# Optimization experiments

Measured on AMD Instinct MI355X. Metric: run time of the kernel, lower is better.

Reference implementation:

```python
import jax, jax.numpy as jnp
import numpy as np

B, L, D, T = 32, 512, 1024, 256
MAX_MENTION_LEN = 10
NEG_INF = float('-inf')


def _static_bounds_and_keep():
    # Full (start, end) grid, flattened row-major like torch's .view(-1, 2)
    s = np.repeat(np.arange(L), L)
    e = np.tile(np.arange(L), L)
    bounds = np.stack([s, e], axis=-1)            # [L*L, 2]
    keep = (e - s) <= MAX_MENTION_LEN             # static per-position mask
    idx = np.nonzero(keep)[0]
    return jnp.asarray(bounds[keep], jnp.int32), jnp.asarray(idx, jnp.int32)


def setup_inputs() -> dict:
    key = jax.random.key(0)
    k0, k1, k2 = jax.random.split(key, 3)
    text_encodings = jax.random.normal(k0, (B, L, D), dtype=jnp.float32)
    mask_ctxt = jnp.ones((B, L), dtype=jnp.int32)
    # word -> wordpiece mapping: [start, end_exclusive); values kept in [1, L)
    tokens_mapping = jax.random.randint(k1, (B, T, 2), 1, L).astype(jnp.int32)
    W = jax.random.normal(k2, (D, 3), dtype=jnp.float32) * 0.02
    b = jnp.zeros((3,), dtype=jnp.float32)
    return {"text_encodings": text_encodings, "mask_ctxt": mask_ctxt,
            "tokens_mapping": tokens_mapping, "W": W, "b": b}


def reference(text_encodings, mask_ctxt, tokens_mapping, W, b):
    # per-token start / end / mention logits
    logits = jnp.einsum('bld,dk->blk', text_encodings, W) + b  # [B, L, 3]
    valid_tok = (mask_ctxt == 1)
    start_lp = jnp.where(valid_tok, logits[:, :, 0], NEG_INF)
    end_lp = jnp.where(valid_tok, logits[:, :, 1], NEG_INF)
    mention_lp = jnp.where(valid_tok, logits[:, :, 2], NEG_INF)

    # scores[b, s, e] = start[b, s] + end[b, e] + sum_{i=s..e} mention[b, i]
    scores = start_lp[:, :, None] + end_lp[:, None, :]          # [B, L, L]
    csum = jnp.cumsum(mention_lp, axis=1)                        # [B, L]
    csum_prev = jnp.concatenate(
        [jnp.zeros((csum.shape[0], 1), csum.dtype), csum[:, :-1]], axis=1)
    scores = scores + (csum[:, None, :] - csum_prev[:, :, None])

    # mention_sizes > 0  <=>  e >= s
    pos = jnp.arange(L)
    size_ok = pos[None, :, None] <= pos[None, None, :]           # [1, L, L]

    # token-boundary masks (scatter 1 at word starts / ends, zero col 0)
    bidx = jnp.arange(tokens_mapping.shape[0])[:, None]
    ts = jnp.zeros(mask_ctxt.shape, jnp.int32).at[bidx, tokens_mapping[:, :, 0]].set(1)
    ts = ts.at[:, 0].set(0)
    te = jnp.zeros(mask_ctxt.shape, jnp.int32).at[bidx, tokens_mapping[:, :, 1] - 1].set(1)
    te = te.at[:, 0].set(0)
    vse = ts[:, :, None] * te[:, None, :]                        # bmm outer product

    valid = size_ok & (mask_ctxt[:, :, None] > 0) & (vse > 0)
    scores = jnp.where(valid, scores, NEG_INF)

    scores_flat = scores.reshape(scores.shape[0], -1)            # [B, L*L]
    bounds_keep, keep_idx = _static_bounds_and_keep()
    out_scores = scores_flat[:, keep_idx]                        # [B, K]
    out_bounds = jnp.broadcast_to(bounds_keep[None],
                                  (scores.shape[0],) + bounds_keep.shape)
    return out_scores, out_bounds
```

## Files before the change

kernel.cpp:

```cpp
#include <hip/hip_runtime.h>
#include <math.h>

#define BB 32
#define LL 512
#define DD 1024
#define TT 256
#define NK 136393
#define NK_LIN 131273
#define S_LIN 502
#define NEG_BIG  -3.0e38f
#define NEG_MASK -1.0e30f

__global__ __launch_bounds__(256) void logits_kernel(
    const float* __restrict__ text, const float* __restrict__ W,
    const float* __restrict__ bias, float* __restrict__ logits)
{
    const int wid  = threadIdx.x >> 6;
    const int lane = threadIdx.x & 63;
    const int row  = blockIdx.x * 4 + wid;
    const float4* t4 = (const float4*)(text + (size_t)row * DD);

    float a0 = 0.f, a1 = 0.f, a2 = 0.f;
#pragma unroll
    for (int j = 0; j < 4; ++j) {
        const int fi = lane + j * 64;
        float4 v = t4[fi];
        const float* wp = W + (size_t)fi * 12;
        a0 += v.x * wp[0];  a1 += v.x * wp[1];  a2 += v.x * wp[2];
        a0 += v.y * wp[3];  a1 += v.y * wp[4];  a2 += v.y * wp[5];
        a0 += v.z * wp[6];  a1 += v.z * wp[7];  a2 += v.z * wp[8];
        a0 += v.w * wp[9];  a1 += v.w * wp[10]; a2 += v.w * wp[11];
    }
#pragma unroll
    for (int off = 32; off; off >>= 1) {
        a0 += __shfl_down(a0, off);
        a1 += __shfl_down(a1, off);
        a2 += __shfl_down(a2, off);
    }
    if (lane == 0) {
        logits[(size_t)row * 3 + 0] = a0 + bias[0];
        logits[(size_t)row * 3 + 1] = a1 + bias[1];
        logits[(size_t)row * 3 + 2] = a2 + bias[2];
    }
}

__global__ __launch_bounds__(512) void scan_kernel(
    const float* __restrict__ logits, const int* __restrict__ mask,
    const int* __restrict__ tmap,
    float* __restrict__ slp, float* __restrict__ elp,
    float* __restrict__ csum, float* __restrict__ cprev,
    int* __restrict__ fs, int* __restrict__ fe)
{
    const int b = blockIdx.x;
    const int l = threadIdx.x;
    __shared__ float sc[LL];
    __shared__ int tsl[LL];
    __shared__ int tel[LL];

    tsl[l] = 0; tel[l] = 0;

    const int idx = b * LL + l;
    const int m = mask[idx];
    const float l0 = logits[(size_t)idx * 3 + 0];
    const float l1 = logits[(size_t)idx * 3 + 1];
    const float l2 = logits[(size_t)idx * 3 + 2];
    const float s_lp = (m == 1) ? l0 : NEG_MASK;
    const float e_lp = (m == 1) ? l1 : NEG_MASK;
    const float m_lp = (m == 1) ? l2 : NEG_MASK;
    sc[l] = m_lp;
    __syncthreads();

    if (l < TT) {
        int s0 = tmap[((size_t)b * TT + l) * 2 + 0];
        int e0 = tmap[((size_t)b * TT + l) * 2 + 1] - 1;
        s0 = min(max(s0, 0), LL - 1);
        e0 = min(max(e0, 0), LL - 1);
        tsl[s0] = 1;
        tel[e0] = 1;
    }

    for (int off = 1; off < LL; off <<= 1) {
        float v = 0.f;
        if (l >= off) v = sc[l - off];
        __syncthreads();
        if (l >= off) sc[l] += v;
        __syncthreads();
    }

    const float cs = sc[l];
    const float cp = (l == 0) ? 0.f : sc[l - 1];

    slp[idx]   = s_lp;
    elp[idx]   = e_lp;
    csum[idx]  = cs;
    cprev[idx] = cp;
    fs[idx] = (l != 0 && m == 1 && tsl[l]) ? 1 : 0;
    fe[idx] = (l != 0 && tel[l]) ? 1 : 0;
}

__global__ __launch_bounds__(256) void out_kernel(
    const float* __restrict__ slp, const float* __restrict__ elp,
    const float* __restrict__ csum, const float* __restrict__ cprev,
    const int* __restrict__ fs, const int* __restrict__ fe,
    float* __restrict__ out)
{
    const int k = blockIdx.x * 256 + threadIdx.x;
    const int b = blockIdx.y;
    if (k >= NK) return;

    int s, e;
    if (k >= NK_LIN) {
        const int r = k - NK_LIN;
        s = S_LIN + (r >> 9);
        e = r & 511;
    } else {
        float f = sqrtf(8.0f * (float)k + 441.0f);
        s = (int)((f - 21.0f) * 0.5f);
        if (s < 0) s = 0;
        if (s > 501) s = 501;
        while ((s + 1) * (s + 22) / 2 <= k) ++s;
        while (s * (s + 21) / 2 > k) --s;
        e = k - s * (s + 21) / 2;
    }

    const int is = b * LL + s;
    const int ie = b * LL + e;
    const bool valid = (s <= e) && fs[is] && fe[ie];
    const float score = valid
        ? ((slp[is] + elp[ie]) + (csum[ie] - cprev[is]))
        : NEG_BIG;

    out[(size_t)b * NK + k] = score;

    float2* bptr = (float2*)(out + (size_t)BB * NK);
    bptr[(size_t)b * NK + k] = make_float2((float)s, (float)e);
}

extern "C" void kernel_launch(void* const* d_in, const int* in_sizes, int n_in,
                              void* d_out, int out_size, void* d_ws, size_t ws_size,
                              hipStream_t stream) {
    const float* text = (const float*)d_in[0];
    const int*   mask = (const int*)d_in[1];
    const int*   tmap = (const int*)d_in[2];
    const float* W    = (const float*)d_in[3];
    const float* bias = (const float*)d_in[4];
    float* out = (float*)d_out;

    float* logits = (float*)d_ws;
    float* slp    = logits + (size_t)BB * LL * 3;
    float* elp    = slp    + (size_t)BB * LL;
    float* csum   = elp    + (size_t)BB * LL;
    float* cprev  = csum   + (size_t)BB * LL;
    int*   fs     = (int*)(cprev + (size_t)BB * LL);
    int*   fe     = fs + (size_t)BB * LL;

    logits_kernel<<<BB * LL / 4, 256, 0, stream>>>(text, W, bias, logits);
    scan_kernel<<<BB, 512, 0, stream>>>(logits, mask, tmap, slp, elp, csum, cprev, fs, fe);
    dim3 g3((NK + 255) / 256, BB);
    out_kernel<<<g3, 256, 0, stream>>>(slp, elp, csum, cprev, fs, fe, out);
}
```

Baseline: 31.52 us.

## Fold scan stage into logits kernel and sum mention logits directly per span

Removes the separate scan kernel. The first 32 blocks of the logits kernel now also build the token start/end boundary flags. Instead of a prefix sum, the output kernel sums mention logits over s..e (at most 11 terms) for valid spans only. This drops one kernel launch and the serial block scan, in exchange for short per-thread loops over valid spans and different floating-point summation order.

```diff
diff --git a/kernel.cpp b/kernel.cpp
--- a/kernel.cpp
+++ b/kernel.cpp
@@ -13,13 +13,33 @@
 
 __global__ __launch_bounds__(256) void logits_kernel(
     const float* __restrict__ text, const float* __restrict__ W,
-    const float* __restrict__ bias, float* __restrict__ logits)
+    const float* __restrict__ bias, const int* __restrict__ mask,
+    const int* __restrict__ tmap,
+    float* __restrict__ slp, float* __restrict__ elp, float* __restrict__ mlp,
+    int* __restrict__ fs, int* __restrict__ fe)
 {
+    __shared__ int tsl[LL];
+    __shared__ int tel[LL];
     const int wid  = threadIdx.x >> 6;
     const int lane = threadIdx.x & 63;
     const int row  = blockIdx.x * 4 + wid;
+    const int b    = blockIdx.x;
+    const int t    = threadIdx.x;
+
+    if (b < BB) {
+        tsl[t] = 0; tsl[t + 256] = 0;
+        tel[t] = 0; tel[t + 256] = 0;
+        __syncthreads();
+        int s0 = tmap[((size_t)b * TT + t) * 2 + 0];
+        int e0 = tmap[((size_t)b * TT + t) * 2 + 1] - 1;
+        s0 = min(max(s0, 0), LL - 1);
+        e0 = min(max(e0, 0), LL - 1);
+        tsl[s0] = 1;
+        tel[e0] = 1;
+        __syncthreads();
+    }
+
     const float4* t4 = (const float4*)(text + (size_t)row * DD);
-
     float a0 = 0.f, a1 = 0.f, a2 = 0.f;
 #pragma unroll
     for (int j = 0; j < 4; ++j) {
@@ -38,69 +58,24 @@
         a2 += __shfl_down(a2, off);
     }
     if (lane == 0) {
-        logits[(size_t)row * 3 + 0] = a0 + bias[0];
-        logits[(size_t)row * 3 + 1] = a1 + bias[1];
-        logits[(size_t)row * 3 + 2] = a2 + bias[2];
-    }
-}
-
-__global__ __launch_bounds__(512) void scan_kernel(
-    const float* __restrict__ logits, const int* __restrict__ mask,
-    const int* __restrict__ tmap,
-    float* __restrict__ slp, float* __restrict__ elp,
-    float* __restrict__ csum, float* __restrict__ cprev,
-    int* __restrict__ fs, int* __restrict__ fe)
-{
-    const int b = blockIdx.x;
-    const int l = threadIdx.x;
-    __shared__ float sc[LL];
-    __shared__ int tsl[LL];
-    __shared__ int tel[LL];
-
-    tsl[l] = 0; tel[l] = 0;
-
-    const int idx = b * LL + l;
-    const int m = mask[idx];
-    const float l0 = logits[(size_t)idx * 3 + 0];
-    const float l1 = logits[(size_t)idx * 3 + 1];
-    const float l2 = logits[(size_t)idx * 3 + 2];
-    const float s_lp = (m == 1) ? l0 : NEG_MASK;
-    const float e_lp = (m == 1) ? l1 : NEG_MASK;
-    const float m_lp = (m == 1) ? l2 : NEG_MASK;
-    sc[l] = m_lp;
-    __syncthreads();
-
-    if (l < TT) {
-        int s0 = tmap[((size_t)b * TT + l) * 2 + 0];
-        int e0 = tmap[((size_t)b * TT + l) * 2 + 1] - 1;
-        s0 = min(max(s0, 0), LL - 1);
-        e0 = min(max(e0, 0), LL - 1);
-        tsl[s0] = 1;
-        tel[e0] = 1;
+        const int m = mask[row];
+        slp[row] = (m == 1) ? a0 + bias[0] : NEG_MASK;
+        elp[row] = (m == 1) ? a1 + bias[1] : NEG_MASK;
+        mlp[row] = (m == 1) ? a2 + bias[2] : NEG_MASK;
     }
 
-    for (int off = 1; off < LL; off <<= 1) {
-        float v = 0.f;
-        if (l >= off) v = sc[l - off];
-        __syncthreads();
-        if (l >= off) sc[l] += v;
-        __syncthreads();
+    if (b < BB) {
+        const int i0 = b * LL + t, i1 = i0 + 256;
+        fs[i0] = (t != 0 && mask[i0] == 1 && tsl[t]) ? 1 : 0;
+        fs[i1] = (mask[i1] == 1 && tsl[t + 256]) ? 1 : 0;
+        fe[i0] = (t != 0 && tel[t]) ? 1 : 0;
+        fe[i1] = tel[t + 256] ? 1 : 0;
     }
-
-    const float cs = sc[l];
-    const float cp = (l == 0) ? 0.f : sc[l - 1];
-
-    slp[idx]   = s_lp;
-    elp[idx]   = e_lp;
-    csum[idx]  = cs;
-    cprev[idx] = cp;
-    fs[idx] = (l != 0 && m == 1 && tsl[l]) ? 1 : 0;
-    fe[idx] = (l != 0 && tel[l]) ? 1 : 0;
 }
 
 __global__ __launch_bounds__(256) void out_kernel(
     const float* __restrict__ slp, const float* __restrict__ elp,
-    const float* __restrict__ csum, const float* __restrict__ cprev,
+    const float* __restrict__ mlp,
     const int* __restrict__ fs, const int* __restrict__ fe,
     float* __restrict__ out)
 {
@@ -123,12 +98,13 @@
         e = k - s * (s + 21) / 2;
     }
 
-    const int is = b * LL + s;
-    const int ie = b * LL + e;
-    const bool valid = (s <= e) && fs[is] && fe[ie];
-    const float score = valid
-        ? ((slp[is] + elp[ie]) + (csum[ie] - cprev[is]))
-        : NEG_BIG;
+    const int base = b * LL;
+    float score = NEG_BIG;
+    if (s <= e && fs[base + s] && fe[base + e]) {
+        float w = 0.f;
+        for (int l = s; l <= e; ++l) w += mlp[base + l];
+        score = (slp[base + s] + elp[base + e]) + w;
+    }
 
     out[(size_t)b * NK + k] = score;
 
@@ -146,16 +122,14 @@
     const float* bias = (const float*)d_in[4];
     float* out = (float*)d_out;
 
-    float* logits = (float*)d_ws;
-    float* slp    = logits + (size_t)BB * LL * 3;
-    float* elp    = slp    + (size_t)BB * LL;
-    float* csum   = elp    + (size_t)BB * LL;
-    float* cprev  = csum   + (size_t)BB * LL;
-    int*   fs     = (int*)(cprev + (size_t)BB * LL);
-    int*   fe     = fs + (size_t)BB * LL;
+    float* slp = (float*)d_ws;
+    float* elp = slp + (size_t)BB * LL;
+    float* mlp = elp + (size_t)BB * LL;
+    int*   fs  = (int*)(mlp + (size_t)BB * LL);
+    int*   fe  = fs + (size_t)BB * LL;
 
-    logits_kernel<<<BB * LL / 4, 256, 0, stream>>>(text, W, bias, logits);
-    scan_kernel<<<BB, 512, 0, stream>>>(logits, mask, tmap, slp, elp, csum, cprev, fs, fe);
+    logits_kernel<<<BB * LL / 4, 256, 0, stream>>>(text, W, bias, mask, tmap,
+                                                   slp, elp, mlp, fs, fe);
     dim3 g3((NK + 255) / 256, BB);
-    out_kernel<<<g3, 256, 0, stream>>>(slp, elp, csum, cprev, fs, fe, out);
+    out_kernel<<<g3, 256, 0, stream>>>(slp, elp, mlp, fs, fe, out);
 }
```

After: 31.82 us. Within noise of the previous version (+0.9%).
